# Kernel tuning notes

Measured on AMD Instinct MI355X. Metric: run time of the kernel, lower is better.

## Reference

```python
import jax, jax.numpy as jnp
import numpy as np

N, NFEAT, NHID, NCLASS, NHEADS = 4096, 512, 64, 40, 8
ALPHA = 0.2
NEG = -9e15


def setup_inputs() -> dict:
    key = jax.random.key(0)
    ks = jax.random.split(key, 6)
    x = jax.random.normal(ks[0], (N, NFEAT), dtype=jnp.float32)
    adj = jax.random.randint(ks[1], (2, N, N), 0, 2, dtype=jnp.int32)
    # Xavier-ish scaled params
    W1 = jax.random.normal(ks[2], (NHEADS, NFEAT, NHID), dtype=jnp.float32) * (1.0 / np.sqrt(NFEAT))
    a1 = jax.random.normal(ks[3], (NHEADS, 2, NHID), dtype=jnp.float32) * (1.0 / np.sqrt(2 * NHID))
    Wo = jax.random.normal(ks[4], (NHEADS * NHID, NCLASS), dtype=jnp.float32) * (1.0 / np.sqrt(NHEADS * NHID))
    ao = jax.random.normal(ks[5], (2, NCLASS), dtype=jnp.float32) * (1.0 / np.sqrt(2 * NCLASS))
    return {"x": x, "adj": adj, "W1": W1, "a1": a1, "Wo": Wo, "ao": ao}


def _gat_layer(h, adj_mask, W, a_src, a_dst, concat):
    # h: [N,F]; W: [...,F,F']; a_src/a_dst: [...,F']
    if W.ndim == 3:  # multi-head: [H,F,F']
        Wh = jnp.einsum('nf,hfd->hnd', h, W)              # [H,N,F']
        f1 = jnp.einsum('hnd,hd->hn', Wh, a_src)           # [H,N]
        f2 = jnp.einsum('hnd,hd->hn', Wh, a_dst)
        e = jax.nn.leaky_relu(f1[:, :, None] + f2[:, None, :], ALPHA)  # [H,N,N]
        e = jnp.where(adj_mask[None], e, NEG)
        att = jax.nn.softmax(e, axis=-1)
        out = jnp.einsum('hnm,hmd->hnd', att, Wh)          # [H,N,F']
    else:
        Wh = h @ W                                         # [N,F']
        f1 = Wh @ a_src
        f2 = Wh @ a_dst
        e = jax.nn.leaky_relu(f1[:, None] + f2[None, :], ALPHA)
        e = jnp.where(adj_mask, e, NEG)
        att = jax.nn.softmax(e, axis=-1)
        out = att @ Wh
    return jax.nn.elu(out) if concat else out


def reference(x, adj, W1, a1, Wo, ao):
    adj1 = adj[1] > 0
    adj0 = adj[0] > 0
    # layer 1: NHEADS heads, concat=True
    h = _gat_layer(x, adj1, W1, a1[:, 0], a1[:, 1], concat=True)   # [H,N,NHID]
    h = jnp.transpose(h, (1, 0, 2)).reshape(x.shape[0], -1)        # [N, H*NHID]
    # output layer: concat=False, then outer ELU + log_softmax
    out = _gat_layer(h, adj0, Wo, ao[0], ao[1], concat=False)      # [N, NCLASS]
    out = jax.nn.elu(out)
    return jax.nn.log_softmax(out, axis=1)
```

## Files before the change

kernel.cpp:

```cpp
#include <hip/hip_runtime.h>
#include <hip/hip_bf16.h>

#define N      4096
#define NFEAT  512
#define NHID   64
#define NHEADS 8
#define NCLASS 40
#define ALPHA  0.2f
#define LOG2E  1.44269504f

typedef unsigned short u16;
typedef unsigned int   u32;
typedef __attribute__((ext_vector_type(8))) short bf16x8;
typedef __attribute__((ext_vector_type(4))) float f32x4;

__device__ __forceinline__ float b2f(u16 u) {
    return __uint_as_float(((u32)u) << 16);
}
__device__ __forceinline__ u32 rnd_hi(float f) {
    u32 u = __float_as_uint(f);
    return u + 0x7FFFu + ((u >> 16) & 1u);
}
__device__ __forceinline__ u32 pk2(float lo, float hi) {
    __hip_bfloat162 h = __float22bfloat162_rn(make_float2(lo, hi));
    return *(u32*)&h;
}
__device__ __forceinline__ u16 f2b(float f) {
    return (u16)(rnd_hi(f) >> 16);
}
__device__ __forceinline__ float mexp(int m, float t) {
    return m ? __builtin_amdgcn_exp2f(fmaxf(t, ALPHA * t)) : 0.f;
}

__global__ __launch_bounds__(256) void kcx(const float* __restrict__ x,
                                           u16* __restrict__ xb) {
    const int g = blockIdx.x * 256 + threadIdx.x;
    const size_t base = (size_t)g * 8;
    float4 v0 = *(const float4*)&x[base];
    float4 v1 = *(const float4*)&x[base + 4];
    uint4 o;
    o.x = pk2(v0.x, v0.y); o.y = pk2(v0.z, v0.w);
    o.z = pk2(v1.x, v1.y); o.w = pk2(v1.z, v1.w);
    *(uint4*)&xb[base] = o;
}

__global__ __launch_bounds__(256) void kcw(const float* __restrict__ W1,
                                           u16* __restrict__ W1b) {
    __shared__ float ts[64 * 68];
    const int t  = threadIdx.x;
    const int f0 = blockIdx.x * 64;
    const int h  = blockIdx.y;
    #pragma unroll
    for (int i = 0; i < 4; ++i) {
        int flat = t + 256 * i;
        int row = flat >> 4;
        int c4  = (flat & 15) * 4;
        *(float4*)&ts[row * 68 + c4] =
            *(const float4*)&W1[((size_t)h * 512 + f0 + row) * 64 + c4];
    }
    __syncthreads();
    const int d  = t >> 2;
    const int fs = (t & 3) * 16;
    u32 p[8];
    #pragma unroll
    for (int j = 0; j < 8; ++j)
        p[j] = pk2(ts[(fs + 2 * j) * 68 + d], ts[(fs + 2 * j + 1) * 68 + d]);
    u32* dst = (u32*)&W1b[((size_t)(h * 64 + d)) * 512 + f0 + fs];
    *(uint4*)dst       = make_uint4(p[0], p[1], p[2], p[3]);
    *(uint4*)(dst + 4) = make_uint4(p[4], p[5], p[6], p[7]);
}

__global__ __launch_bounds__(256, 4) void k1m_gemm1(const u16* __restrict__ xb,
                                                    const u16* __restrict__ W1b,
                                                    u16* __restrict__ Wh1T) {
    __shared__ u16 xs[64 * 72];
    __shared__ u16 wvs[64 * 72];
    const int t    = threadIdx.x;
    const int n0   = blockIdx.x * 64;
    const int h    = blockIdx.y;
    const int lane = t & 63;
    const int l15  = lane & 15;
    const int q    = lane >> 4;
    const int wrow = (t >> 6) * 16;
    f32x4 acc[4];
    #pragma unroll
    for (int df = 0; df < 4; ++df)
        #pragma unroll
        for (int r = 0; r < 4; ++r) acc[df][r] = 0.f;
    for (int f0 = 0; f0 < 512; f0 += 64) {
        uint4 sx[2], sw[2];
        #pragma unroll
        for (int i = 0; i < 2; ++i) {
            int flat = t + 256 * i;
            int row = flat >> 3;
            int c8  = (flat & 7) * 8;
            sx[i] = *(const uint4*)&xb[(size_t)(n0 + row) * 512 + f0 + c8];
            sw[i] = *(const uint4*)&W1b[((size_t)(h * 64 + row)) * 512 + f0 + c8];
        }
        __syncthreads();
        #pragma unroll
        for (int i = 0; i < 2; ++i) {
            int flat = t + 256 * i;
            int row = flat >> 3;
            int c8  = (flat & 7) * 8;
            *(uint4*)&xs[row * 72 + c8]  = sx[i];
            *(uint4*)&wvs[row * 72 + c8] = sw[i];
        }
        __syncthreads();
        #pragma unroll
        for (int ks = 0; ks < 2; ++ks) {
            int k0 = ks * 32 + q * 8;
            bf16x8 a = *(const bf16x8*)&xs[(wrow + l15) * 72 + k0];
            #pragma unroll
            for (int df = 0; df < 4; ++df) {
                bf16x8 b = *(const bf16x8*)&wvs[(df * 16 + l15) * 72 + k0];
                acc[df] = __builtin_amdgcn_mfma_f32_16x16x32_bf16(a, b, acc[df], 0, 0, 0);
            }
        }
    }
    #pragma unroll
    for (int df = 0; df < 4; ++df) {
        uint2 o;
        o.x = pk2(acc[df][0], acc[df][1]);
        o.y = pk2(acc[df][2], acc[df][3]);
        *(uint2*)&Wh1T[((size_t)(h * 64 + df * 16 + l15)) * 4096 + n0 + wrow + q * 4] = o;
    }
}

__global__ __launch_bounds__(256) void k2_f12(const u16* __restrict__ Wh1T,
                                              const float* __restrict__ a1,
                                              float* __restrict__ F1,
                                              float* __restrict__ F2) {
    const int g = blockIdx.x * 256 + threadIdx.x;
    const int h = g >> 12;
    const int n = g & 4095;
    float s1 = 0.f, s2 = 0.f;
    #pragma unroll 8
    for (int d = 0; d < 64; ++d) {
        float v = b2f(Wh1T[((size_t)(h * 64 + d)) * 4096 + n]);
        s1 += v * a1[h * 128 + d];
        s2 += v * a1[h * 128 + 64 + d];
    }
    F1[h * 4096 + n] = s1 * LOG2E;
    F2[h * 4096 + n] = s2 * LOG2E;
}

__global__ __launch_bounds__(256, 4) void k3_attn1(const int* __restrict__ adj1,
                                                   const u16* __restrict__ Wh1T,
                                                   const float* __restrict__ F1,
                                                   const float* __restrict__ F2,
                                                   float* __restrict__ pacc1,
                                                   float* __restrict__ pz1) {
    __shared__ u16  wbf[64 * 136];
    __shared__ u16  whT[80 * 136];
    __shared__ float f1s[64];
    const int t     = threadIdx.x;
    const int n0    = blockIdx.x * 64;
    const int h     = blockIdx.y;
    const int chunk = blockIdx.z;
    const int lane  = t & 63;
    const int l15   = lane & 15;
    const int q     = lane >> 4;
    const int wrow  = (t >> 6) * 16;
    const int c4    = (t & 31) * 4;
    const int rg    = t >> 5;
    if (t < 64) f1s[t] = F1[h * N + n0 + t];
    #pragma unroll
    for (int i = 0; i < 9; ++i) {
        int flat = t + 256 * i;
        if (flat < 16 * 136) {
            int row = 64 + flat / 136;
            whT[row * 136 + (flat % 136)] = (row == 64) ? (u16)0x3F80 : (u16)0;
        }
    }
    f32x4 acc[5];
    #pragma unroll
    for (int df = 0; df < 5; ++df)
        #pragma unroll
        for (int r = 0; r < 4; ++r) acc[df][r] = 0.f;

    const int mbeg = chunk * 2048;
    int4 aprev[8];
    #pragma unroll
    for (int i = 0; i < 8; ++i)
        aprev[i] = *(const int4*)&adj1[(size_t)(n0 + rg + 8 * i) * N + mbeg + c4];
    __syncthreads();

    for (int m0 = mbeg; m0 < mbeg + 2048; m0 += 128) {
        float4 F2v = *(const float4*)&F2[h * N + m0 + c4];
        #pragma unroll
        for (int i = 0; i < 8; ++i) {
            int rr = rg + 8 * i;
            int4 a4 = aprev[i];
            float f1v = f1s[rr];
            float w0 = mexp(a4.x, f1v + F2v.x);
            float w1 = mexp(a4.y, f1v + F2v.y);
            float w2 = mexp(a4.z, f1v + F2v.z);
            float w3 = mexp(a4.w, f1v + F2v.w);
            uint2 pk;
            pk.x = pk2(w0, w1);
            pk.y = pk2(w2, w3);
            *(uint2*)&wbf[rr * 136 + c4] = pk;
        }
        int mn = (m0 + 128 < mbeg + 2048) ? m0 + 128 : mbeg;
        #pragma unroll
        for (int i = 0; i < 8; ++i)
            aprev[i] = *(const int4*)&adj1[(size_t)(n0 + rg + 8 * i) * N + mn + c4];
        #pragma unroll
        for (int i = 0; i < 4; ++i) {
            int flat = t + 256 * i;
            int row = flat >> 4;
            int c8  = (flat & 15) * 8;
            *(uint4*)&whT[row * 136 + c8] =
                *(const uint4*)&Wh1T[((size_t)(h * 64 + row)) * 4096 + m0 + c8];
        }
        __syncthreads();
        #pragma unroll
        for (int ks = 0; ks < 4; ++ks) {
            int k0 = ks * 32 + q * 8;
            bf16x8 a = *(const bf16x8*)&wbf[(wrow + l15) * 136 + k0];
            #pragma unroll
            for (int df = 0; df < 5; ++df) {
                bf16x8 b = *(const bf16x8*)&whT[(df * 16 + l15) * 136 + k0];
                acc[df] = __builtin_amdgcn_mfma_f32_16x16x32_bf16(a, b, acc[df], 0, 0, 0);
            }
        }
        __syncthreads();
    }
    const size_t rowbase = (size_t)(chunk * 8 + h) * 4096 + n0;
    #pragma unroll
    for (int r = 0; r < 4; ++r) {
        int nl = wrow + q * 4 + r;
        float z = __shfl(acc[4][r], lane & 48);
        if (l15 == 0) pz1[rowbase + nl] = z;
        #pragma unroll
        for (int df = 0; df < 4; ++df)
            pacc1[(rowbase + nl) * 64 + df * 16 + l15] = acc[df][r];
    }
}

__global__ __launch_bounds__(256) void k3b_norm(const float* __restrict__ pacc1,
                                                const float* __restrict__ pz1,
                                                float* __restrict__ h1) {
    const int g = blockIdx.x * 256 + threadIdx.x;
    const int d = g & 63;
    const int h = (g >> 6) & 7;
    const int n = g >> 9;
    const size_t i0 = (size_t)h * 4096 + n;
    float s = pacc1[i0 * 64 + d] + pacc1[(i0 + 8 * 4096) * 64 + d];
    float z = pz1[i0] + pz1[i0 + 8 * 4096];
    float v = s / fmaxf(z, 1e-30f);
    h1[(size_t)n * 512 + h * 64 + d] = v > 0.f ? v : __expf(v) - 1.f;
}

__global__ __launch_bounds__(256) void k4_gemm2(const float* __restrict__ h1,
                                                const float* __restrict__ Wo,
                                                float* __restrict__ Wh2) {
    const int t = threadIdx.x;
    const int c = t & 63;
    const int n = blockIdx.x * 4 + (t >> 6);
    if (c < NCLASS) {
        const float* hrow = &h1[(size_t)n * 512];
        float acc = 0.f;
        #pragma unroll 8
        for (int f = 0; f < 512; ++f)
            acc += hrow[f] * Wo[f * NCLASS + c];
        Wh2[(size_t)n * NCLASS + c] = acc;
    }
}

__global__ __launch_bounds__(256) void k4b_fo(const float* __restrict__ Wh2,
                                              const float* __restrict__ ao,
                                              float* __restrict__ F1o,
                                              float* __restrict__ F2o,
                                              u16* __restrict__ Wh2T) {
    const int n = blockIdx.x * 256 + threadIdx.x;
    float s1 = 0.f, s2 = 0.f;
    #pragma unroll
    for (int c = 0; c < NCLASS; ++c) {
        float v = Wh2[(size_t)n * NCLASS + c];
        s1 += v * ao[c];
        s2 += v * ao[NCLASS + c];
        Wh2T[(size_t)c * 4096 + n] = f2b(v);
    }
    F1o[n] = s1 * LOG2E;
    F2o[n] = s2 * LOG2E;
}

__global__ __launch_bounds__(256, 4) void k5a_attn2(const int* __restrict__ adj0,
                                                    const u16* __restrict__ Wh2T,
                                                    const float* __restrict__ F1o,
                                                    const float* __restrict__ F2o,
                                                    float* __restrict__ pacc,
                                                    float* __restrict__ pz) {
    __shared__ u16  wbf[64 * 136];
    __shared__ u16  whT[64 * 136];
    __shared__ float f1s[64];
    const int t     = threadIdx.x;
    const int n0    = blockIdx.x * 64;
    const int chunk = blockIdx.y;
    const int mbase = chunk * 256;
    const int lane  = t & 63;
    const int l15   = lane & 15;
    const int q     = lane >> 4;
    const int wrow  = (t >> 6) * 16;
    const int c4    = (t & 31) * 4;
    const int rg    = t >> 5;
    if (t < 64) f1s[t] = F1o[n0 + t];
    #pragma unroll
    for (int i = 0; i < 13; ++i) {
        int flat = t + 256 * i;
        if (flat < 24 * 136) {
            int row = 40 + flat / 136;
            whT[row * 136 + (flat % 136)] = (row == 48) ? (u16)0x3F80 : (u16)0;
        }
    }
    f32x4 acc[4];
    #pragma unroll
    for (int df = 0; df < 4; ++df)
        #pragma unroll
        for (int r = 0; r < 4; ++r) acc[df][r] = 0.f;
    int4 aprev[8];
    #pragma unroll
    for (int i = 0; i < 8; ++i)
        aprev[i] = *(const int4*)&adj0[(size_t)(n0 + rg + 8 * i) * N + mbase + c4];
    __syncthreads();

    for (int mt = 0; mt < 2; ++mt) {
        int m0 = mbase + mt * 128;
        float4 F2v = *(const float4*)&F2o[m0 + c4];
        #pragma unroll
        for (int i = 0; i < 8; ++i) {
            int rr = rg + 8 * i;
            int4 a4 = aprev[i];
            float f1v = f1s[rr];
            float w0 = mexp(a4.x, f1v + F2v.x);
            float w1 = mexp(a4.y, f1v + F2v.y);
            float w2 = mexp(a4.z, f1v + F2v.z);
            float w3 = mexp(a4.w, f1v + F2v.w);
            uint2 pk;
            pk.x = pk2(w0, w1);
            pk.y = pk2(w2, w3);
            *(uint2*)&wbf[rr * 136 + c4] = pk;
        }
        int mn = mbase + ((mt + 1) & 1) * 128;
        #pragma unroll
        for (int i = 0; i < 8; ++i)
            aprev[i] = *(const int4*)&adj0[(size_t)(n0 + rg + 8 * i) * N + mn + c4];
        #pragma unroll
        for (int i = 0; i < 3; ++i) {
            int flat = t + 256 * i;
            if (flat < 640) {
                int row = flat >> 4;
                int c8  = (flat & 15) * 8;
                *(uint4*)&whT[row * 136 + c8] =
                    *(const uint4*)&Wh2T[(size_t)row * 4096 + m0 + c8];
            }
        }
        __syncthreads();
        #pragma unroll
        for (int ks = 0; ks < 4; ++ks) {
            int k0 = ks * 32 + q * 8;
            bf16x8 a = *(const bf16x8*)&wbf[(wrow + l15) * 136 + k0];
            #pragma unroll
            for (int df = 0; df < 4; ++df) {
                bf16x8 b = *(const bf16x8*)&whT[(df * 16 + l15) * 136 + k0];
                acc[df] = __builtin_amdgcn_mfma_f32_16x16x32_bf16(a, b, acc[df], 0, 0, 0);
            }
        }
        __syncthreads();
    }
    #pragma unroll
    for (int r = 0; r < 4; ++r) {
        int n = n0 + wrow + q * 4 + r;
        float z = __shfl(acc[3][r], lane & 48);
        if (l15 == 0) pz[(size_t)chunk * N + n] = z;
        #pragma unroll
        for (int df = 0; df < 3; ++df) {
            int c = df * 16 + l15;
            if (c < NCLASS)
                pacc[((size_t)chunk * N + n) * NCLASS + c] = acc[df][r];
        }
    }
}

__global__ __launch_bounds__(256) void k5b_final(const float* __restrict__ pacc,
                                                 const float* __restrict__ pz,
                                                 float* __restrict__ out) {
    const int t = threadIdx.x;
    const int lane = t & 63;
    const int n = blockIdx.x * 4 + (t >> 6);
    float s = 0.f, Z = 0.f;
    #pragma unroll
    for (int ch = 0; ch < 16; ++ch) {
        Z += pz[(size_t)ch * N + n];
        if (lane < NCLASS) s += pacc[(size_t)(ch * N + n) * NCLASS + lane];
    }
    float v;
    if (lane < NCLASS) {
        v = s / fmaxf(Z, 1e-30f);
        v = v > 0.f ? v : __expf(v) - 1.f;
    } else {
        v = -INFINITY;
    }
    float mx = v;
    #pragma unroll
    for (int off = 32; off >= 1; off >>= 1) mx = fmaxf(mx, __shfl_xor(mx, off));
    float ex = (lane < NCLASS) ? __expf(v - mx) : 0.f;
    #pragma unroll
    for (int off = 32; off >= 1; off >>= 1) ex += __shfl_xor(ex, off);
    float lse = mx + __logf(ex);
    if (lane < NCLASS) out[(size_t)n * NCLASS + lane] = v - lse;
}

extern "C" void kernel_launch(void* const* d_in, const int* in_sizes, int n_in,
                              void* d_out, int out_size, void* d_ws, size_t ws_size,
                              hipStream_t stream) {
    const float* x   = (const float*)d_in[0];
    const int*   adj = (const int*)d_in[1];
    const float* W1  = (const float*)d_in[2];
    const float* a1  = (const float*)d_in[3];
    const float* Wo  = (const float*)d_in[4];
    const float* ao  = (const float*)d_in[5];

    float* ws    = (float*)d_ws;
    float* h1    = ws;
    float* F1    = h1 + 2097152;
    float* F2    = F1 + 32768;
    float* Wh2   = F2 + 32768;
    float* F1o   = Wh2 + 163840;
    float* F2o   = F1o + 4096;
    float* pz    = F2o + 4096;
    float* pz1   = pz + 65536;
    u16*   Wh1T  = (u16*)(pz1 + 65536);
    u16*   Wh2T  = Wh1T + 2097152;
    float* R     = (float*)(Wh2T + 163840);
    u16*   xb    = (u16*)R;
    u16*   W1b   = xb + 2097152;
    float* pacc1 = R;
    float* pacc  = R;

    const int* adj0 = adj;
    const int* adj1 = adj + (size_t)N * N;

    hipLaunchKernelGGL(kcx,       dim3(1024),     dim3(256), 0, stream, x, xb);
    hipLaunchKernelGGL(kcw,       dim3(8, 8),     dim3(256), 0, stream, W1, W1b);
    hipLaunchKernelGGL(k1m_gemm1, dim3(64, 8),    dim3(256), 0, stream, xb, W1b, Wh1T);
    hipLaunchKernelGGL(k2_f12,    dim3(128),      dim3(256), 0, stream, Wh1T, a1, F1, F2);
    hipLaunchKernelGGL(k3_attn1,  dim3(64, 8, 2), dim3(256), 0, stream, adj1, Wh1T, F1, F2, pacc1, pz1);
    hipLaunchKernelGGL(k3b_norm,  dim3(8192),     dim3(256), 0, stream, pacc1, pz1, h1);
    hipLaunchKernelGGL(k4_gemm2,  dim3(1024),     dim3(256), 0, stream, h1, Wo, Wh2);
    hipLaunchKernelGGL(k4b_fo,    dim3(16),       dim3(256), 0, stream, Wh2, ao, F1o, F2o, Wh2T);
    hipLaunchKernelGGL(k5a_attn2, dim3(64, 16),   dim3(256), 0, stream, adj0, Wh2T, F1o, F2o, pacc, pz);
    hipLaunchKernelGGL(k5b_final, dim3(1024),     dim3(256), 0, stream, pacc, pz, (float*)d_out);
}
```

Before: 347.7 us.

## Fuse attention-logit projections into GEMM epilogues and use register ones-fragment for row sums

Computes F1/F2 in the epilogue of the first GEMM from the fp32 accumulators using lane shuffles, removing the separate k2_f12 pass that re-read Wh1T. Likewise folds the output-layer projection and the bf16 transpose into k4_gemm2, dropping k4b_fo and the fp32 Wh2 buffer. Attention kernels now take the softmax denominator from an MFMA against a constant register fragment of ones instead of an extra shared-memory row, which shrinks LDS use. k5a gets launch bounds of 5 waves per SIMD. F1/F2 now come from unrounded fp32 accumulators rather than bf16, which changes numerics slightly.

Result: faster. 334.8 us (-3.7%).

```diff
diff --git a/kernel.cpp b/kernel.cpp
--- a/kernel.cpp
+++ b/kernel.cpp
@@ -30,6 +30,12 @@
 }
 __device__ __forceinline__ float mexp(int m, float t) {
     return m ? __builtin_amdgcn_exp2f(fmaxf(t, ALPHA * t)) : 0.f;
+}
+__device__ __forceinline__ bf16x8 ones_frag() {
+    union { u16 u[8]; bf16x8 v; } o;
+    #pragma unroll
+    for (int j = 0; j < 8; ++j) o.u[j] = 0x3F80;
+    return o.v;
 }
 
 __global__ __launch_bounds__(256) void kcx(const float* __restrict__ x,
@@ -72,7 +78,10 @@
 
 __global__ __launch_bounds__(256, 4) void k1m_gemm1(const u16* __restrict__ xb,
                                                     const u16* __restrict__ W1b,
-                                                    u16* __restrict__ Wh1T) {
+                                                    const float* __restrict__ a1,
+                                                    u16* __restrict__ Wh1T,
+                                                    float* __restrict__ F1,
+                                                    float* __restrict__ F2) {
     __shared__ u16 xs[64 * 72];
     __shared__ u16 wvs[64 * 72];
     const int t    = threadIdx.x;
@@ -125,24 +134,31 @@
         o.y = pk2(acc[df][2], acc[df][3]);
         *(uint2*)&Wh1T[((size_t)(h * 64 + df * 16 + l15)) * 4096 + n0 + wrow + q * 4] = o;
     }
-}
-
-__global__ __launch_bounds__(256) void k2_f12(const u16* __restrict__ Wh1T,
-                                              const float* __restrict__ a1,
-                                              float* __restrict__ F1,
-                                              float* __restrict__ F2) {
-    const int g = blockIdx.x * 256 + threadIdx.x;
-    const int h = g >> 12;
-    const int n = g & 4095;
-    float s1 = 0.f, s2 = 0.f;
-    #pragma unroll 8
-    for (int d = 0; d < 64; ++d) {
-        float v = b2f(Wh1T[((size_t)(h * 64 + d)) * 4096 + n]);
-        s1 += v * a1[h * 128 + d];
-        s2 += v * a1[h * 128 + 64 + d];
-    }
-    F1[h * 4096 + n] = s1 * LOG2E;
-    F2[h * 4096 + n] = s2 * LOG2E;
+    float a1v[4], a2v[4];
+    #pragma unroll
+    for (int df = 0; df < 4; ++df) {
+        a1v[df] = a1[h * 128 + df * 16 + l15];
+        a2v[df] = a1[h * 128 + 64 + df * 16 + l15];
+    }
+    #pragma unroll
+    for (int r = 0; r < 4; ++r) {
+        float s1 = 0.f, s2 = 0.f;
+        #pragma unroll
+        for (int df = 0; df < 4; ++df) {
+            s1 += acc[df][r] * a1v[df];
+            s2 += acc[df][r] * a2v[df];
+        }
+        #pragma unroll
+        for (int off = 8; off >= 1; off >>= 1) {
+            s1 += __shfl_xor(s1, off);
+            s2 += __shfl_xor(s2, off);
+        }
+        if (l15 == 0) {
+            int n = n0 + wrow + q * 4 + r;
+            F1[h * 4096 + n] = s1 * LOG2E;
+            F2[h * 4096 + n] = s2 * LOG2E;
+        }
+    }
 }
 
 __global__ __launch_bounds__(256, 4) void k3_attn1(const int* __restrict__ adj1,
@@ -152,7 +168,7 @@
                                                    float* __restrict__ pacc1,
                                                    float* __restrict__ pz1) {
     __shared__ u16  wbf[64 * 136];
-    __shared__ u16  whT[80 * 136];
+    __shared__ u16  whT[64 * 136];
     __shared__ float f1s[64];
     const int t     = threadIdx.x;
     const int n0    = blockIdx.x * 64;
@@ -164,15 +180,8 @@
     const int wrow  = (t >> 6) * 16;
     const int c4    = (t & 31) * 4;
     const int rg    = t >> 5;
+    const bf16x8 bones = ones_frag();
     if (t < 64) f1s[t] = F1[h * N + n0 + t];
-    #pragma unroll
-    for (int i = 0; i < 9; ++i) {
-        int flat = t + 256 * i;
-        if (flat < 16 * 136) {
-            int row = 64 + flat / 136;
-            whT[row * 136 + (flat % 136)] = (row == 64) ? (u16)0x3F80 : (u16)0;
-        }
-    }
     f32x4 acc[5];
     #pragma unroll
     for (int df = 0; df < 5; ++df)
@@ -220,10 +229,11 @@
             int k0 = ks * 32 + q * 8;
             bf16x8 a = *(const bf16x8*)&wbf[(wrow + l15) * 136 + k0];
             #pragma unroll
-            for (int df = 0; df < 5; ++df) {
+            for (int df = 0; df < 4; ++df) {
                 bf16x8 b = *(const bf16x8*)&whT[(df * 16 + l15) * 136 + k0];
                 acc[df] = __builtin_amdgcn_mfma_f32_16x16x32_bf16(a, b, acc[df], 0, 0, 0);
             }
+            acc[4] = __builtin_amdgcn_mfma_f32_16x16x32_bf16(a, bones, acc[4], 0, 0, 0);
         }
         __syncthreads();
     }
@@ -231,8 +241,7 @@
     #pragma unroll
     for (int r = 0; r < 4; ++r) {
         int nl = wrow + q * 4 + r;
-        float z = __shfl(acc[4][r], lane & 48);
-        if (l15 == 0) pz1[rowbase + nl] = z;
+        if (l15 == 0) pz1[rowbase + nl] = acc[4][r];
         #pragma unroll
         for (int df = 0; df < 4; ++df)
             pacc1[(rowbase + nl) * 64 + df * 16 + l15] = acc[df][r];
@@ -255,46 +264,42 @@
 
 __global__ __launch_bounds__(256) void k4_gemm2(const float* __restrict__ h1,
                                                 const float* __restrict__ Wo,
-                                                float* __restrict__ Wh2) {
+                                                const float* __restrict__ ao,
+                                                float* __restrict__ F1o,
+                                                float* __restrict__ F2o,
+                                                u16* __restrict__ Wh2T) {
     const int t = threadIdx.x;
     const int c = t & 63;
     const int n = blockIdx.x * 4 + (t >> 6);
+    float acc = 0.f;
     if (c < NCLASS) {
         const float* hrow = &h1[(size_t)n * 512];
-        float acc = 0.f;
         #pragma unroll 8
         for (int f = 0; f < 512; ++f)
             acc += hrow[f] * Wo[f * NCLASS + c];
-        Wh2[(size_t)n * NCLASS + c] = acc;
-    }
-}
-
-__global__ __launch_bounds__(256) void k4b_fo(const float* __restrict__ Wh2,
-                                              const float* __restrict__ ao,
-                                              float* __restrict__ F1o,
-                                              float* __restrict__ F2o,
-                                              u16* __restrict__ Wh2T) {
-    const int n = blockIdx.x * 256 + threadIdx.x;
-    float s1 = 0.f, s2 = 0.f;
-    #pragma unroll
-    for (int c = 0; c < NCLASS; ++c) {
-        float v = Wh2[(size_t)n * NCLASS + c];
-        s1 += v * ao[c];
-        s2 += v * ao[NCLASS + c];
-        Wh2T[(size_t)c * 4096 + n] = f2b(v);
-    }
-    F1o[n] = s1 * LOG2E;
-    F2o[n] = s2 * LOG2E;
-}
-
-__global__ __launch_bounds__(256, 4) void k5a_attn2(const int* __restrict__ adj0,
+        Wh2T[(size_t)c * 4096 + n] = f2b(acc);
+    }
+    float s1 = (c < NCLASS) ? acc * ao[c] : 0.f;
+    float s2 = (c < NCLASS) ? acc * ao[NCLASS + c] : 0.f;
+    #pragma unroll
+    for (int off = 32; off >= 1; off >>= 1) {
+        s1 += __shfl_xor(s1, off);
+        s2 += __shfl_xor(s2, off);
+    }
+    if (c == 0) {
+        F1o[n] = s1 * LOG2E;
+        F2o[n] = s2 * LOG2E;
+    }
+}
+
+__global__ __launch_bounds__(256, 5) void k5a_attn2(const int* __restrict__ adj0,
                                                     const u16* __restrict__ Wh2T,
                                                     const float* __restrict__ F1o,
                                                     const float* __restrict__ F2o,
                                                     float* __restrict__ pacc,
                                                     float* __restrict__ pz) {
     __shared__ u16  wbf[64 * 136];
-    __shared__ u16  whT[64 * 136];
+    __shared__ u16  whT[48 * 136];
     __shared__ float f1s[64];
     const int t     = threadIdx.x;
     const int n0    = blockIdx.x * 64;
@@ -306,14 +311,12 @@
     const int wrow  = (t >> 6) * 16;
     const int c4    = (t & 31) * 4;
     const int rg    = t >> 5;
+    const bf16x8 bones = ones_frag();
     if (t < 64) f1s[t] = F1o[n0 + t];
     #pragma unroll
-    for (int i = 0; i < 13; ++i) {
-        int flat = t + 256 * i;
-        if (flat < 24 * 136) {
-            int row = 40 + flat / 136;
-            whT[row * 136 + (flat % 136)] = (row == 48) ? (u16)0x3F80 : (u16)0;
-        }
+    for (int i = 0; i < 5; ++i) {
+        int idx = t + 256 * i;
+        if (idx < 1088) whT[40 * 136 + idx] = 0;
     }
     f32x4 acc[4];
     #pragma unroll
@@ -363,18 +366,18 @@
             int k0 = ks * 32 + q * 8;
             bf16x8 a = *(const bf16x8*)&wbf[(wrow + l15) * 136 + k0];
             #pragma unroll
-            for (int df = 0; df < 4; ++df) {
+            for (int df = 0; df < 3; ++df) {
                 bf16x8 b = *(const bf16x8*)&whT[(df * 16 + l15) * 136 + k0];
                 acc[df] = __builtin_amdgcn_mfma_f32_16x16x32_bf16(a, b, acc[df], 0, 0, 0);
             }
+            acc[3] = __builtin_amdgcn_mfma_f32_16x16x32_bf16(a, bones, acc[3], 0, 0, 0);
         }
         __syncthreads();
     }
     #pragma unroll
     for (int r = 0; r < 4; ++r) {
         int n = n0 + wrow + q * 4 + r;
-        float z = __shfl(acc[3][r], lane & 48);
-        if (l15 == 0) pz[(size_t)chunk * N + n] = z;
+        if (l15 == 0) pz[(size_t)chunk * N + n] = acc[3][r];
         #pragma unroll
         for (int df = 0; df < 3; ++df) {
             int c = df * 16 + l15;
@@ -427,8 +430,7 @@
     float* h1    = ws;
     float* F1    = h1 + 2097152;
     float* F2    = F1 + 32768;
-    float* Wh2   = F2 + 32768;
-    float* F1o   = Wh2 + 163840;
+    float* F1o   = F2 + 32768;
     float* F2o   = F1o + 4096;
     float* pz    = F2o + 4096;
     float* pz1   = pz + 65536;
@@ -445,12 +447,10 @@
 
     hipLaunchKernelGGL(kcx,       dim3(1024),     dim3(256), 0, stream, x, xb);
     hipLaunchKernelGGL(kcw,       dim3(8, 8),     dim3(256), 0, stream, W1, W1b);
-    hipLaunchKernelGGL(k1m_gemm1, dim3(64, 8),    dim3(256), 0, stream, xb, W1b, Wh1T);
-    hipLaunchKernelGGL(k2_f12,    dim3(128),      dim3(256), 0, stream, Wh1T, a1, F1, F2);
+    hipLaunchKernelGGL(k1m_gemm1, dim3(64, 8),    dim3(256), 0, stream, xb, W1b, a1, Wh1T, F1, F2);
     hipLaunchKernelGGL(k3_attn1,  dim3(64, 8, 2), dim3(256), 0, stream, adj1, Wh1T, F1, F2, pacc1, pz1);
     hipLaunchKernelGGL(k3b_norm,  dim3(8192),     dim3(256), 0, stream, pacc1, pz1, h1);
-    hipLaunchKernelGGL(k4_gemm2,  dim3(1024),     dim3(256), 0, stream, h1, Wo, Wh2);
-    hipLaunchKernelGGL(k4b_fo,    dim3(16),       dim3(256), 0, stream, Wh2, ao, F1o, F2o, Wh2T);
+    hipLaunchKernelGGL(k4_gemm2,  dim3(1024),     dim3(256), 0, stream, h1, Wo, ao, F1o, F2o, Wh2T);
     hipLaunchKernelGGL(k5a_attn2, dim3(64, 16),   dim3(256), 0, stream, adj0, Wh2T, F1o, F2o, pacc, pz);
     hipLaunchKernelGGL(k5b_final, dim3(1024),     dim3(256), 0, stream, pacc, pz, (float*)d_out);
 }
```
